# Kernel tuning notes

Measured on AMD Instinct MI355X. Metric: run time of the kernel, lower is better.

Reference implementation:

```python
import jax, jax.numpy as jnp
import numpy as np

N_NODES = 100000
N_EDGES = 1600000
D_IN, D_HID, D_OUT = 32, 16, 2


def graph_conv(x, edge_index, w_rel, w_root, b):
    # PyG GraphConv (aggr='add'): out_i = x_i @ W_root^T + (sum_{j in N(i)} x_j) @ W_rel^T + b
    src, dst = edge_index[0], edge_index[1]
    msgs = x[src]                                            # [E, d] neighbor gather
    agg = jax.ops.segment_sum(msgs, dst, num_segments=N_NODES)  # [N, d] scatter-add
    return agg @ w_rel.T + x @ w_root.T + b


def setup_inputs() -> dict:
    key = jax.random.key(0)
    ks = jax.random.split(key, 8)
    x = jax.random.normal(ks[0], (N_NODES, D_IN), dtype=jnp.float32)
    edge_index = jax.random.randint(ks[1], (2, N_EDGES), 0, N_NODES, dtype=jnp.int64)
    def glorot(k, shape):
        lim = np.sqrt(6.0 / (shape[0] + shape[1]))
        return jax.random.uniform(k, shape, jnp.float32, -lim, lim)
    w1_rel = glorot(ks[2], (D_HID, D_IN))
    w1_root = glorot(ks[3], (D_HID, D_IN))
    b1 = jnp.zeros((D_HID,), jnp.float32)
    w2_rel = glorot(ks[4], (D_OUT, D_HID))
    w2_root = glorot(ks[5], (D_OUT, D_HID))
    b2 = jnp.zeros((D_OUT,), jnp.float32)
    return {"x": x, "edge_index": edge_index,
            "w1_rel": w1_rel, "w1_root": w1_root, "b1": b1,
            "w2_rel": w2_rel, "w2_root": w2_root, "b2": b2}


def reference(x, edge_index, w1_rel, w1_root, b1, w2_rel, w2_root, b2):
    h = graph_conv(x, edge_index, w1_rel, w1_root, b1)
    h = jax.nn.relu(h)
    out = graph_conv(h, edge_index, w2_rel, w2_root, b2)
    return out
```

## Files before the change

kernel.cpp:

```cpp
#include <hip/hip_runtime.h>

#define N_NODES 100000
#define N_EDGES 1600000
#define D_IN 32
#define D_HID 16
#define D_OUT 2

#define NPB 128
#define NB 782
#define NROWS (NB * NPB)
#define CHUNK 6400
#define BBLOCKS 250
#define EPT 13

#define PBC 2560
#define DUMMY_SRC 100000u
#define DUMMY_REC ((127u << 17) | DUMMY_SRC)


__device__ __forceinline__ unsigned bfr(float x) {
    unsigned u = __float_as_uint(x);
    return (u + 0x7FFFu + ((u >> 16) & 1u)) >> 16;
}
__device__ __forceinline__ float bfu(unsigned lo16) {
    return __uint_as_float(lo16 << 16);
}

__global__ __launch_bounds__(512) void k_bin_node1(
    const int* __restrict__ ei, const float* __restrict__ x,
    const float* __restrict__ w_rel, const float* __restrict__ w_root,
    const float* __restrict__ bb,
    unsigned short* __restrict__ xr, float* __restrict__ agg,
    int* __restrict__ gcur, unsigned* __restrict__ recs2)
{
    __shared__ int cnt[NB];
    __shared__ int loff[NB];
    __shared__ int gbase[NB];
    __shared__ unsigned sorted[CHUNK];
    __shared__ unsigned short bkt16[CHUNK];
    __shared__ float s_rel[D_HID * D_IN];
    __shared__ float s_root[D_HID * D_IN];
    __shared__ float s_b[D_HID];
    int blk = blockIdx.x, tid = threadIdx.x;
    int e0 = blk * CHUNK;

    int srcs[EPT], dsts[EPT];
#pragma unroll
    for (int k = 0; k < EPT; k++) {
        int off = tid + k * 512;
        bool ok = off < CHUNK;
        int e = e0 + off;
        srcs[k] = ok ? ei[e] : 0;
        dsts[k] = ok ? ei[N_EDGES + e] : -1;
    }

    for (int i = tid; i < D_HID * D_IN; i += 512) {
        s_rel[i]  = w_rel[i];
        s_root[i] = w_root[i];
    }
    if (tid < D_HID) s_b[tid] = bb[tid];
    for (int i = tid; i < NB; i += 512) cnt[i] = 0;
    __syncthreads();

    int rank[EPT];
#pragma unroll
    for (int k = 0; k < EPT; k++)
        rank[k] = (dsts[k] >= 0) ? atomicAdd(&cnt[dsts[k] >> 7], 1) : 0;

    int node = blk * 512 + tid;
    if (node == N_NODES) {
        uint4* xp = (uint4*)(xr + (size_t)node * D_HID);
        xp[0] = make_uint4(0, 0, 0, 0);
        xp[1] = make_uint4(0, 0, 0, 0);
    } else if (node < N_NODES) {
        float row[D_IN];
        const float4* xp = (const float4*)(x + (size_t)node * D_IN);
#pragma unroll
        for (int i = 0; i < D_IN / 4; i++) {
            float4 v = xp[i];
            row[4*i+0] = v.x; row[4*i+1] = v.y; row[4*i+2] = v.z; row[4*i+3] = v.w;
        }
        float oa[D_HID], orr[D_HID];
#pragma unroll
        for (int o = 0; o < D_HID; o++) {
            float a = 0.f, r = s_b[o];
#pragma unroll
            for (int k = 0; k < D_IN; k++) {
                a += row[k] * s_rel[o * D_IN + k];
                r += row[k] * s_root[o * D_IN + k];
            }
            oa[o] = a; orr[o] = r;
        }
        unsigned p[8];
#pragma unroll
        for (int i = 0; i < 8; i++)
            p[i] = bfr(oa[2*i]) | (bfr(oa[2*i+1]) << 16);
        uint4* xrp = (uint4*)(xr + (size_t)node * D_HID);
        xrp[0] = make_uint4(p[0], p[1], p[2], p[3]);
        xrp[1] = make_uint4(p[4], p[5], p[6], p[7]);
        float4* aggp = (float4*)(agg + (size_t)node * D_HID);
#pragma unroll
        for (int i = 0; i < D_HID / 4; i++)
            aggp[i] = make_float4(orr[4*i], orr[4*i+1], orr[4*i+2], orr[4*i+3]);
    }
    __syncthreads();

    if (tid < 64) {
        int running = 0;
        for (int c = 0; c < (NB + 63) / 64; c++) {
            int idx = c * 64 + tid;
            int v = (idx < NB) ? cnt[idx] : 0;
            int incl = v;
#pragma unroll
            for (int off = 1; off < 64; off <<= 1) {
                int t = __shfl_up(incl, off);
                if (tid >= off) incl += t;
            }
            if (idx < NB) loff[idx] = running + incl - v;
            running += __shfl(incl, 63);
        }
    } else {
        for (int i = tid - 64; i < NB; i += 448)
            gbase[i] = (cnt[i] > 0) ? atomicAdd(&gcur[i], cnt[i]) : 0;
    }
    __syncthreads();

#pragma unroll
    for (int k = 0; k < EPT; k++) {
        if (dsts[k] >= 0) {
            int bkt = dsts[k] >> 7;
            int p = loff[bkt] + rank[k];
            sorted[p] = ((unsigned)(dsts[k] & (NPB - 1)) << 17) | (unsigned)srcs[k];
            bkt16[p] = (unsigned short)bkt;
        }
    }
    __syncthreads();

    for (int i = tid; i < CHUNK; i += 512) {
        int b = bkt16[i];
        int idx = gbase[b] + (i - loff[b]);
        if (idx < PBC)
            recs2[b * PBC + idx] = sorted[i];
    }
}

__global__ __launch_bounds__(512) void k_sortacc(
    const int* __restrict__ gcur, unsigned* __restrict__ recs2,
    const unsigned short* __restrict__ srcf, const float* __restrict__ agg,
    const float* __restrict__ w_rel2, const float* __restrict__ w_root2,
    const float* __restrict__ bb2,
    float* __restrict__ hr, float* __restrict__ outv,
    unsigned* __restrict__ bbase)
{
    __shared__ unsigned stage[PBC];
    __shared__ unsigned sorted[PBC];
    __shared__ int hist[NPB], base[NPB];
    __shared__ float s_rel2[D_OUT * D_HID];
    __shared__ float s_root2[D_OUT * D_HID];
    __shared__ float s_b2[D_OUT];
    int b = blockIdx.x, tid = threadIdx.x;
    int n = min(gcur[b], PBC);
    unsigned* w = recs2 + (size_t)b * PBC;

    int t = tid >> 2, l = tid & 3;
    int node = b * NPB + t;
    float acc0 = 0.f, acc1 = 0.f, acc2_ = 0.f, acc3 = 0.f;
    if (node < N_NODES) {
        const float4 r4 = *(const float4*)(agg + (size_t)node * D_HID + l * 4);
        acc0 = r4.x; acc1 = r4.y; acc2_ = r4.z; acc3 = r4.w;
    }

    if (tid < D_OUT * D_HID) {
        s_rel2[tid]  = w_rel2[tid];
        s_root2[tid] = w_root2[tid];
    }
    if (tid < D_OUT) s_b2[tid] = bb2[tid];

    if (tid < NPB) hist[tid] = 0;
    for (int i = tid; i < n; i += 512) stage[i] = w[i];
    __syncthreads();

    unsigned rc[PBC / 512];
    int rk[PBC / 512];
#pragma unroll
    for (int j = 0; j < PBC / 512; j++) {
        int i = tid + j * 512;
        if (i < n) {
            rc[j] = stage[i];
            rk[j] = atomicAdd(&hist[rc[j] >> 17], 1);
        } else {
            rc[j] = DUMMY_REC; rk[j] = -1;
        }
    }
    __syncthreads();

    if (tid < 64) {
        int v0 = hist[tid], v1 = hist[tid + 64];
        int s0 = v0, s1 = v1;
#pragma unroll
        for (int off = 1; off < 64; off <<= 1) {
            int t0 = __shfl_up(s0, off);
            int t1 = __shfl_up(s1, off);
            if (tid >= off) { s0 += t0; s1 += t1; }
        }
        int tot0 = __shfl(s0, 63);
        base[tid]      = s0 - v0;
        base[tid + 64] = tot0 + s1 - v1;
    }
    __syncthreads();

#pragma unroll
    for (int j = 0; j < PBC / 512; j++) {
        if (rk[j] >= 0)
            sorted[base[rc[j] >> 17] + rk[j]] = rc[j];
    }
    __syncthreads();

    for (int i = tid; i < n; i += 512) w[i] = sorted[i];
    if (tid < NPB)
        bbase[b * NPB + tid] = (unsigned)base[tid] | ((unsigned)hist[tid] << 16);

    int cbase = base[t], c = hist[t];
    for (int r0 = 0; r0 < c; r0 += 8) {
        int m = c - r0;
        uint2 vv[8];
#pragma unroll
        for (int j = 0; j < 8; j++) {
            unsigned src = (j < m) ? (sorted[cbase + r0 + j] & 0x1FFFF) : DUMMY_SRC;
            vv[j] = *(const uint2*)(srcf + (size_t)src * D_HID + l * 4);
        }
#pragma unroll
        for (int j = 0; j < 8; j++) {
            acc0 += bfu(vv[j].x & 0xFFFFu); acc1 += bfu(vv[j].x >> 16);
            acc2_ += bfu(vv[j].y & 0xFFFFu); acc3 += bfu(vv[j].y >> 16);
        }
    }

    float h0 = fmaxf(acc0, 0.f), h1 = fmaxf(acc1, 0.f);
    float h2 = fmaxf(acc2_, 0.f), h3 = fmaxf(acc3, 0.f);
    float pr[D_OUT], pp[D_OUT];
#pragma unroll
    for (int o = 0; o < D_OUT; o++) {
        const float* wr = &s_rel2[o * D_HID + l * 4];
        const float* wo = &s_root2[o * D_HID + l * 4];
        pr[o] = h0 * wr[0] + h1 * wr[1] + h2 * wr[2] + h3 * wr[3];
        pp[o] = h0 * wo[0] + h1 * wo[1] + h2 * wo[2] + h3 * wo[3];
    }
#pragma unroll
    for (int m = 1; m < 4; m <<= 1) {
        pr[0] += __shfl_xor(pr[0], m); pr[1] += __shfl_xor(pr[1], m);
        pp[0] += __shfl_xor(pp[0], m); pp[1] += __shfl_xor(pp[1], m);
    }
    if (l == 0) {
        if (node < N_NODES) {
            ((float2*)hr)[node]   = make_float2(pr[0], pr[1]);
            ((float2*)outv)[node] = make_float2(pp[0] + s_b2[0], pp[1] + s_b2[1]);
        } else if (node == N_NODES) {
            ((float2*)hr)[node] = make_float2(0.f, 0.f);
        }
    }
}

__global__ __launch_bounds__(256) void k_acc2(
    const unsigned* __restrict__ recs2, const unsigned* __restrict__ bbase,
    const float* __restrict__ hr, float* __restrict__ outv)
{
    __shared__ unsigned srt[PBC];
    int b = blockIdx.x, tid = threadIdx.x;
    unsigned pk127 = bbase[b * NPB + 127];
    int n = (int)(pk127 & 0xFFFFu) + (int)(pk127 >> 16);
    const unsigned* rp = recs2 + (size_t)b * PBC;
    for (int i = tid; i < n; i += 256) srt[i] = rp[i];

    int t = tid >> 1, l = tid & 1;
    unsigned pk = bbase[b * NPB + t];
    int cbase = (int)(pk & 0xFFFFu), c = (int)(pk >> 16);
    int node = b * NPB + t;
    __syncthreads();

    float acc = 0.f;
    for (int r0 = 0; r0 < c; r0 += 8) {
        int m = c - r0;
        float vv[8];
#pragma unroll
        for (int j = 0; j < 8; j++) {
            unsigned src = (j < m) ? (srt[cbase + r0 + j] & 0x1FFFF) : DUMMY_SRC;
            vv[j] = hr[(size_t)src * D_OUT + l];
        }
#pragma unroll
        for (int j = 0; j < 8; j++) acc += vv[j];
    }
    if (node < N_NODES)
        outv[(size_t)node * D_OUT + l] += acc;
}

extern "C" void kernel_launch(void* const* d_in, const int* in_sizes, int n_in,
                              void* d_out, int out_size, void* d_ws, size_t ws_size,
                              hipStream_t stream) {
    const float* x       = (const float*)d_in[0];
    const int*   ei      = (const int*)  d_in[1];
    const float* w1_rel  = (const float*)d_in[2];
    const float* w1_root = (const float*)d_in[3];
    const float* b1      = (const float*)d_in[4];
    const float* w2_rel  = (const float*)d_in[5];
    const float* w2_root = (const float*)d_in[6];
    const float* b2      = (const float*)d_in[7];
    float* out = (float*)d_out;

    float*          agg   = (float*)d_ws;
    unsigned short* xrh   = (unsigned short*)(agg + (size_t)NROWS * D_HID);
    unsigned*       recs2 = (unsigned*)(xrh + (size_t)NROWS * D_HID);
    float*          hr    = (float*)(recs2 + (size_t)NB * PBC);
    unsigned*       bbase = (unsigned*)(hr + (size_t)NROWS * D_OUT);
    int*            gcur  = (int*)(bbase + (size_t)NROWS);

    hipMemsetAsync(gcur, 0, NB * sizeof(int), stream);

    k_bin_node1<<<dim3(BBLOCKS), dim3(512), 0, stream>>>(
        ei, x, w1_rel, w1_root, b1, xrh, agg, gcur, recs2);

    k_sortacc<<<dim3(NB), dim3(512), 0, stream>>>(
        gcur, recs2, xrh, agg, w2_rel, w2_root, b2, hr, out, bbase);

    k_acc2<<<dim3(NB), dim3(256), 0, stream>>>(recs2, bbase, hr, out);
}
```

Measured before the change: 133.9 us.

## Fuse layer-2 sort/accumulate and second aggregation into one cooperative kernel

Merges the sort+accumulate kernel and the second-layer aggregation kernel into a single cooperative launch with 256-thread blocks, using a grid-wide sync between the two phases. The sorted records stay in shared memory across the sync, so the kernel no longer writes the sorted records and per-node base/count array back to global memory and reloads them. This removes one kernel launch and that global round trip. In exchange it relies on all 782 blocks being co-resident (launch_bounds 256,4) and pays for a grid barrier. Each thread now handles two nodes in phase one.

```diff
diff --git a/kernel.cpp b/kernel.cpp
--- a/kernel.cpp
+++ b/kernel.cpp
@@ -1,4 +1,6 @@
 #include <hip/hip_runtime.h>
+#include <hip/hip_cooperative_groups.h>
+namespace cg = cooperative_groups;
 
 #define N_NODES 100000
 #define N_EDGES 1600000
@@ -144,13 +146,12 @@
     }
 }
 
-__global__ __launch_bounds__(512) void k_sortacc(
-    const int* __restrict__ gcur, unsigned* __restrict__ recs2,
+__global__ __launch_bounds__(256, 4) void k_sortacc2(
+    const int* __restrict__ gcur, const unsigned* __restrict__ recs2,
     const unsigned short* __restrict__ srcf, const float* __restrict__ agg,
     const float* __restrict__ w_rel2, const float* __restrict__ w_root2,
     const float* __restrict__ bb2,
-    float* __restrict__ hr, float* __restrict__ outv,
-    unsigned* __restrict__ bbase)
+    float* __restrict__ hr, float* __restrict__ outv)
 {
     __shared__ unsigned stage[PBC];
     __shared__ unsigned sorted[PBC];
@@ -160,31 +161,22 @@
     __shared__ float s_b2[D_OUT];
     int b = blockIdx.x, tid = threadIdx.x;
     int n = min(gcur[b], PBC);
-    unsigned* w = recs2 + (size_t)b * PBC;
-
-    int t = tid >> 2, l = tid & 3;
-    int node = b * NPB + t;
-    float acc0 = 0.f, acc1 = 0.f, acc2_ = 0.f, acc3 = 0.f;
-    if (node < N_NODES) {
-        const float4 r4 = *(const float4*)(agg + (size_t)node * D_HID + l * 4);
-        acc0 = r4.x; acc1 = r4.y; acc2_ = r4.z; acc3 = r4.w;
-    }
+    const unsigned* w = recs2 + (size_t)b * PBC;
 
     if (tid < D_OUT * D_HID) {
         s_rel2[tid]  = w_rel2[tid];
         s_root2[tid] = w_root2[tid];
     }
     if (tid < D_OUT) s_b2[tid] = bb2[tid];
-
     if (tid < NPB) hist[tid] = 0;
-    for (int i = tid; i < n; i += 512) stage[i] = w[i];
-    __syncthreads();
-
-    unsigned rc[PBC / 512];
-    int rk[PBC / 512];
-#pragma unroll
-    for (int j = 0; j < PBC / 512; j++) {
-        int i = tid + j * 512;
+    for (int i = tid; i < n; i += 256) stage[i] = w[i];
+    __syncthreads();
+
+    unsigned rc[PBC / 256];
+    int rk[PBC / 256];
+#pragma unroll
+    for (int j = 0; j < PBC / 256; j++) {
+        int i = tid + j * 256;
         if (i < n) {
             rc[j] = stage[i];
             rk[j] = atomicAdd(&hist[rc[j] >> 17], 1);
@@ -210,88 +202,83 @@
     __syncthreads();
 
 #pragma unroll
-    for (int j = 0; j < PBC / 512; j++) {
+    for (int j = 0; j < PBC / 256; j++) {
         if (rk[j] >= 0)
             sorted[base[rc[j] >> 17] + rk[j]] = rc[j];
     }
     __syncthreads();
 
-    for (int i = tid; i < n; i += 512) w[i] = sorted[i];
-    if (tid < NPB)
-        bbase[b * NPB + tid] = (unsigned)base[tid] | ((unsigned)hist[tid] << 16);
-
-    int cbase = base[t], c = hist[t];
-    for (int r0 = 0; r0 < c; r0 += 8) {
-        int m = c - r0;
-        uint2 vv[8];
+    int t4 = tid >> 2, l = tid & 3;
+#pragma unroll
+    for (int half = 0; half < 2; half++) {
+        int t = t4 + half * 64;
+        int node = b * NPB + t;
+        int cbase = base[t], c = hist[t];
+        float acc0 = 0.f, acc1 = 0.f, acc2_ = 0.f, acc3 = 0.f;
+        if (node < N_NODES) {
+            const float4 r4 = *(const float4*)(agg + (size_t)node * D_HID + l * 4);
+            acc0 = r4.x; acc1 = r4.y; acc2_ = r4.z; acc3 = r4.w;
+        }
+        for (int r0 = 0; r0 < c; r0 += 8) {
+            int m = c - r0;
+            uint2 vv[8];
+#pragma unroll
+            for (int j = 0; j < 8; j++) {
+                unsigned src = (j < m) ? (sorted[cbase + r0 + j] & 0x1FFFF) : DUMMY_SRC;
+                vv[j] = *(const uint2*)(srcf + (size_t)src * D_HID + l * 4);
+            }
+#pragma unroll
+            for (int j = 0; j < 8; j++) {
+                acc0 += bfu(vv[j].x & 0xFFFFu); acc1 += bfu(vv[j].x >> 16);
+                acc2_ += bfu(vv[j].y & 0xFFFFu); acc3 += bfu(vv[j].y >> 16);
+            }
+        }
+
+        float h0 = fmaxf(acc0, 0.f), h1 = fmaxf(acc1, 0.f);
+        float h2 = fmaxf(acc2_, 0.f), h3 = fmaxf(acc3, 0.f);
+        float pr[D_OUT], pp[D_OUT];
+#pragma unroll
+        for (int o = 0; o < D_OUT; o++) {
+            const float* wr = &s_rel2[o * D_HID + l * 4];
+            const float* wo = &s_root2[o * D_HID + l * 4];
+            pr[o] = h0 * wr[0] + h1 * wr[1] + h2 * wr[2] + h3 * wr[3];
+            pp[o] = h0 * wo[0] + h1 * wo[1] + h2 * wo[2] + h3 * wo[3];
+        }
+#pragma unroll
+        for (int m = 1; m < 4; m <<= 1) {
+            pr[0] += __shfl_xor(pr[0], m); pr[1] += __shfl_xor(pr[1], m);
+            pp[0] += __shfl_xor(pp[0], m); pp[1] += __shfl_xor(pp[1], m);
+        }
+        if (l == 0) {
+            if (node < N_NODES) {
+                ((float2*)hr)[node]   = make_float2(pr[0], pr[1]);
+                ((float2*)outv)[node] = make_float2(pp[0] + s_b2[0], pp[1] + s_b2[1]);
+            } else if (node == N_NODES) {
+                ((float2*)hr)[node] = make_float2(0.f, 0.f);
+            }
+        }
+    }
+
+    __threadfence();
+    cg::this_grid().sync();
+
+    int t2 = tid >> 1, l2 = tid & 1;
+    int cbase2 = base[t2], c2 = hist[t2];
+    int node2 = b * NPB + t2;
+    float acc = 0.f;
+    for (int r0 = 0; r0 < c2; r0 += 8) {
+        int m = c2 - r0;
+        float vv[8];
 #pragma unroll
         for (int j = 0; j < 8; j++) {
-            unsigned src = (j < m) ? (sorted[cbase + r0 + j] & 0x1FFFF) : DUMMY_SRC;
-            vv[j] = *(const uint2*)(srcf + (size_t)src * D_HID + l * 4);
-        }
-#pragma unroll
-        for (int j = 0; j < 8; j++) {
-            acc0 += bfu(vv[j].x & 0xFFFFu); acc1 += bfu(vv[j].x >> 16);
-            acc2_ += bfu(vv[j].y & 0xFFFFu); acc3 += bfu(vv[j].y >> 16);
-        }
-    }
-
-    float h0 = fmaxf(acc0, 0.f), h1 = fmaxf(acc1, 0.f);
-    float h2 = fmaxf(acc2_, 0.f), h3 = fmaxf(acc3, 0.f);
-    float pr[D_OUT], pp[D_OUT];
-#pragma unroll
-    for (int o = 0; o < D_OUT; o++) {
-        const float* wr = &s_rel2[o * D_HID + l * 4];
-        const float* wo = &s_root2[o * D_HID + l * 4];
-        pr[o] = h0 * wr[0] + h1 * wr[1] + h2 * wr[2] + h3 * wr[3];
-        pp[o] = h0 * wo[0] + h1 * wo[1] + h2 * wo[2] + h3 * wo[3];
-    }
-#pragma unroll
-    for (int m = 1; m < 4; m <<= 1) {
-        pr[0] += __shfl_xor(pr[0], m); pr[1] += __shfl_xor(pr[1], m);
-        pp[0] += __shfl_xor(pp[0], m); pp[1] += __shfl_xor(pp[1], m);
-    }
-    if (l == 0) {
-        if (node < N_NODES) {
-            ((float2*)hr)[node]   = make_float2(pr[0], pr[1]);
-            ((float2*)outv)[node] = make_float2(pp[0] + s_b2[0], pp[1] + s_b2[1]);
-        } else if (node == N_NODES) {
-            ((float2*)hr)[node] = make_float2(0.f, 0.f);
-        }
-    }
-}
-
-__global__ __launch_bounds__(256) void k_acc2(
-    const unsigned* __restrict__ recs2, const unsigned* __restrict__ bbase,
-    const float* __restrict__ hr, float* __restrict__ outv)
-{
-    __shared__ unsigned srt[PBC];
-    int b = blockIdx.x, tid = threadIdx.x;
-    unsigned pk127 = bbase[b * NPB + 127];
-    int n = (int)(pk127 & 0xFFFFu) + (int)(pk127 >> 16);
-    const unsigned* rp = recs2 + (size_t)b * PBC;
-    for (int i = tid; i < n; i += 256) srt[i] = rp[i];
-
-    int t = tid >> 1, l = tid & 1;
-    unsigned pk = bbase[b * NPB + t];
-    int cbase = (int)(pk & 0xFFFFu), c = (int)(pk >> 16);
-    int node = b * NPB + t;
-    __syncthreads();
-
-    float acc = 0.f;
-    for (int r0 = 0; r0 < c; r0 += 8) {
-        int m = c - r0;
-        float vv[8];
-#pragma unroll
-        for (int j = 0; j < 8; j++) {
-            unsigned src = (j < m) ? (srt[cbase + r0 + j] & 0x1FFFF) : DUMMY_SRC;
-            vv[j] = hr[(size_t)src * D_OUT + l];
+            unsigned src = (j < m) ? (sorted[cbase2 + r0 + j] & 0x1FFFF) : DUMMY_SRC;
+            vv[j] = hr[(size_t)src * D_OUT + l2];
         }
 #pragma unroll
         for (int j = 0; j < 8; j++) acc += vv[j];
     }
-    if (node < N_NODES)
-        outv[(size_t)node * D_OUT + l] += acc;
+    if (node2 < N_NODES)
+        outv[(size_t)node2 * D_OUT + l2] += acc;
 }
 
 extern "C" void kernel_launch(void* const* d_in, const int* in_sizes, int n_in,
@@ -311,16 +298,27 @@
     unsigned short* xrh   = (unsigned short*)(agg + (size_t)NROWS * D_HID);
     unsigned*       recs2 = (unsigned*)(xrh + (size_t)NROWS * D_HID);
     float*          hr    = (float*)(recs2 + (size_t)NB * PBC);
-    unsigned*       bbase = (unsigned*)(hr + (size_t)NROWS * D_OUT);
-    int*            gcur  = (int*)(bbase + (size_t)NROWS);
+    int*            gcur  = (int*)(hr + (size_t)NROWS * D_OUT);
 
     hipMemsetAsync(gcur, 0, NB * sizeof(int), stream);
 
     k_bin_node1<<<dim3(BBLOCKS), dim3(512), 0, stream>>>(
         ei, x, w1_rel, w1_root, b1, xrh, agg, gcur, recs2);
 
-    k_sortacc<<<dim3(NB), dim3(512), 0, stream>>>(
-        gcur, recs2, xrh, agg, w2_rel, w2_root, b2, hr, out, bbase);
-
-    k_acc2<<<dim3(NB), dim3(256), 0, stream>>>(recs2, bbase, hr, out);
-}
+    {
+        const int* a_gcur = gcur;
+        const unsigned* a_recs2 = recs2;
+        const unsigned short* a_srcf = xrh;
+        const float* a_agg = agg;
+        const float* a_wr = w2_rel;
+        const float* a_wo = w2_root;
+        const float* a_b2 = b2;
+        float* a_hr = hr;
+        float* a_out = out;
+        void* args[] = { (void*)&a_gcur, (void*)&a_recs2, (void*)&a_srcf,
+                         (void*)&a_agg, (void*)&a_wr, (void*)&a_wo,
+                         (void*)&a_b2, (void*)&a_hr, (void*)&a_out };
+        hipLaunchCooperativeKernel((const void*)k_sortacc2,
+                                   dim3(NB), dim3(256), args, 0, stream);
+    }
+}
```

After: 288.1 us. 115% more time.
